# Performance work log

Measured on AMD Instinct MI355X. Metric: run time of the kernel, lower is better.

The kernel has to match this reference:

```python
import jax, jax.numpy as jnp
import numpy as np

EPS = 1e-5

def _layernorm(x, gamma, beta):
    mu = jnp.mean(x, axis=-1, keepdims=True)
    var = jnp.mean(jnp.square(x - mu), axis=-1, keepdims=True)
    return (x - mu) * jax.lax.rsqrt(var + EPS) * gamma + beta


def setup_inputs() -> dict:
    key = jax.random.key(0)
    ks = jax.random.split(key, 10)
    B, T, D, D1, F = 16, 256, 256, 64, 1024
    x = jax.random.normal(ks[0], (B, T, D), dtype=jnp.float32)
    U1 = jax.random.normal(ks[1], (B, T, T, D1), dtype=jnp.float32)
    mask = jnp.ones((B, T), dtype=bool)
    s = lambda fan_in: 1.0 / np.sqrt(fan_in)
    return {
        "x": x,
        "U1": U1,
        "mask": mask,
        "ln_mia_g": jnp.ones((D,), jnp.float32),
        "ln_mia_b": jnp.zeros((D,), jnp.float32),
        "Wv": jax.random.normal(ks[2], (D, D1), jnp.float32) * s(D),
        "Wo": jax.random.normal(ks[3], (D1, D), jnp.float32) * s(D1),
        "ln_ffn_g": jnp.ones((D,), jnp.float32),
        "ln_ffn_b": jnp.zeros((D,), jnp.float32),
        "W1": jax.random.normal(ks[4], (D, F), jnp.float32) * s(D),
        "b1": jnp.zeros((F,), jnp.float32),
        "W2": jax.random.normal(ks[5], (F, D), jnp.float32) * s(F),
        "b2": jnp.zeros((D,), jnp.float32),
    }


def reference(x, U1, mask, ln_mia_g, ln_mia_b, Wv, Wo, ln_ffn_g, ln_ffn_b, W1, b1, W2, b2):
    # MIA: per-channel softmax over source tokens j of external logits U1
    x_norm = _layernorm(x, ln_mia_g, ln_mia_b)          # [B,T,D]
    V = jnp.einsum('btd,de->bte', x_norm, Wv)           # [B,T,D1]
    # mask[b,j] False -> suppress source token j for all queries i, channels c
    logits = jnp.where(mask[:, None, :, None], U1, -jnp.inf)  # [B,T,T,D1]
    attn = jax.nn.softmax(logits, axis=2)               # softmax over j
    mia_out = jnp.einsum('bijc,bjc->bic', attn, V)      # [B,T,D1]
    x = x + jnp.einsum('btc,cd->btd', mia_out, Wo)
    # FFN (pre-norm), exact GELU as in torch nn.GELU default
    h = _layernorm(x, ln_ffn_g, ln_ffn_b)
    h = jax.nn.gelu(h @ W1 + b1, approximate=False) @ W2 + b2
    return x + h
```

## Files before the change

kernel.cpp:

```cpp
#include <hip/hip_runtime.h>
#include <math.h>

#define LNEPS 1e-5f

typedef short bf16x8 __attribute__((ext_vector_type(8)));
typedef float f32x4 __attribute__((ext_vector_type(4)));

__device__ __forceinline__ unsigned short f2bf(float f) {
    union { float f; unsigned int u; } v; v.f = f;
    unsigned int r = v.u + 0x7fffu + ((v.u >> 16) & 1u);
    return (unsigned short)(r >> 16);
}

__device__ __forceinline__ void block_ln_stats(float v, int tid, float* red,
                                               float& mu, float& rs) {
    float s = v, ss = v * v;
#pragma unroll
    for (int off = 32; off; off >>= 1) {
        s += __shfl_xor(s, off);
        ss += __shfl_xor(ss, off);
    }
    if ((tid & 63) == 0) { red[tid >> 6] = s; red[4 + (tid >> 6)] = ss; }
    __syncthreads();
    s = red[0] + red[1] + red[2] + red[3];
    ss = red[4] + red[5] + red[6] + red[7];
    mu = s * (1.0f / 256.0f);
    float var = ss * (1.0f / 256.0f) - mu * mu;
    rs = rsqrtf(var + LNEPS);
}

__device__ __forceinline__ float gelu_exact(float v) {
    return 0.5f * v * (1.0f + erff(v * 0.70710678118654752f));
}

__global__ __launch_bounds__(256) void kATT(const float* __restrict__ x,
                                            const float* __restrict__ g,
                                            const float* __restrict__ be,
                                            const float* __restrict__ Wv,
                                            float* __restrict__ V,
                                            const float* __restrict__ W1,
                                            unsigned short* __restrict__ W1t,
                                            const float* __restrict__ W2,
                                            unsigned short* __restrict__ W2t) {
    __shared__ float smem[32 * 33];
    const int bid = blockIdx.x, tid = threadIdx.x;
    if (bid < 4096) {
        float* sx = smem;
        float* red = smem + 256;
        float* part = smem + 264;
        const int token = bid;
        float v = x[(size_t)token * 256 + tid];
        float mu, rs;
        block_ln_stats(v, tid, red, mu, rs);
        sx[tid] = (v - mu) * rs * g[tid] + be[tid];
        __syncthreads();
        const int c = tid & 63, q = tid >> 6;
        float p = 0.f;
        const float* wp = Wv + (size_t)(q * 64) * 64 + c;
#pragma unroll 8
        for (int d = 0; d < 64; ++d) p = fmaf(sx[q * 64 + d], wp[(size_t)d * 64], p);
        part[q * 64 + c] = p;
        __syncthreads();
        if (tid < 64)
            V[(size_t)token * 64 + tid] =
                part[tid] + part[64 + tid] + part[128 + tid] + part[192 + tid];
    } else {
        int b = bid - 4096;
        const float* W;
        unsigned short* Wt;
        int K, N, n0, k0;
        if (b < 256) { W = W1; Wt = W1t; K = 256; N = 1024; n0 = (b & 31) * 32; k0 = (b >> 5) * 32; }
        else { b -= 256; W = W2; Wt = W2t; K = 1024; N = 256; n0 = (b & 7) * 32; k0 = (b >> 3) * 32; }
        float(*s)[33] = (float(*)[33])smem;
        const int cl = tid & 31, rq = tid >> 5;
#pragma unroll
        for (int i = 0; i < 4; ++i)
            s[rq * 4 + i][cl] = W[(size_t)(k0 + rq * 4 + i) * N + n0 + cl];
        __syncthreads();
#pragma unroll
        for (int i = 0; i < 4; ++i)
            Wt[(size_t)(n0 + rq * 4 + i) * K + k0 + cl] = f2bf(s[cl][rq * 4 + i]);
    }
}

__global__ __launch_bounds__(256) void kB(const float* __restrict__ x,
                                          const float4* __restrict__ U4,
                                          const int* __restrict__ mask,
                                          const float4* __restrict__ V4,
                                          const float* __restrict__ Wo,
                                          const float* __restrict__ gf,
                                          const float* __restrict__ bf,
                                          const float* __restrict__ b2,
                                          float* __restrict__ out,
                                          unsigned short* __restrict__ xn2b) {
    __shared__ float sl[16][64], al[16][64];
    __shared__ float mia[64];
    __shared__ float red[8];
    __shared__ float mkf[256];
    const int token = blockIdx.x, tid = threadIdx.x;
    const int b = token >> 8;
    const int l16 = tid & 15, jo = tid >> 4;
    mkf[tid] = (mask[b * 256 + tid] != 0) ? 1.0f : 0.0f;
    __syncthreads();

    float s0 = 0, s1 = 0, s2 = 0, s3 = 0;
    float a0 = 0, a1 = 0, a2 = 0, a3 = 0;
    const size_t ub = (size_t)token * (256 * 16);
    const size_t vb = (size_t)b * (256 * 16);
#pragma unroll 4
    for (int j = jo; j < 256; j += 16) {
        float4 u = U4[ub + (size_t)j * 16 + l16];
        float4 vv = V4[vb + (size_t)j * 16 + l16];
        float mw = mkf[j];
        float w;
        w = __expf(u.x) * mw; s0 += w; a0 = fmaf(w, vv.x, a0);
        w = __expf(u.y) * mw; s1 += w; a1 = fmaf(w, vv.y, a1);
        w = __expf(u.z) * mw; s2 += w; a2 = fmaf(w, vv.z, a2);
        w = __expf(u.w) * mw; s3 += w; a3 = fmaf(w, vv.w, a3);
    }
    sl[jo][l16 * 4 + 0] = s0; sl[jo][l16 * 4 + 1] = s1;
    sl[jo][l16 * 4 + 2] = s2; sl[jo][l16 * 4 + 3] = s3;
    al[jo][l16 * 4 + 0] = a0; al[jo][l16 * 4 + 1] = a1;
    al[jo][l16 * 4 + 2] = a2; al[jo][l16 * 4 + 3] = a3;
    __syncthreads();
    if (tid < 64) {
        float S = 0, A = 0;
#pragma unroll
        for (int p = 0; p < 16; ++p) { S += sl[p][tid]; A += al[p][tid]; }
        mia[tid] = A / S;
    }
    __syncthreads();

    float r = x[(size_t)token * 256 + tid];
#pragma unroll 8
    for (int c = 0; c < 64; ++c) r = fmaf(mia[c], Wo[(size_t)c * 256 + tid], r);
    out[(size_t)token * 256 + tid] = r + b2[tid];
    float mu, rs;
    block_ln_stats(r, tid, red, mu, rs);
    xn2b[(size_t)token * 256 + tid] = f2bf((r - mu) * rs * gf[tid] + bf[tid]);
}

__global__ __launch_bounds__(256) void kC2m(const unsigned short* __restrict__ A,
                                            const unsigned short* __restrict__ Bt,
                                            const float* __restrict__ b1,
                                            unsigned short* __restrict__ Aact) {
    __shared__ __align__(16) unsigned short As[128][72];
    __shared__ __align__(16) unsigned short Bs[64][72];
    const int tid = threadIdx.x;
    const int tileM = blockIdx.y * 128, tileN = blockIdx.x * 64;
    const int w = tid >> 6, lane = tid & 63;
    const int waveM = w >> 1, waveN = w & 1;
    const int fr = lane & 15, fg = lane >> 4;
    f32x4 acc[4][2] = {};
    for (int kc = 0; kc < 256; kc += 64) {
#pragma unroll
        for (int h = 0; h < 4; ++h) {
            int idx = tid + h * 256;
            int row = idx >> 3, seg = idx & 7;
            *(uint4*)&As[row][seg * 8] =
                *(const uint4*)&A[(size_t)(tileM + row) * 256 + kc + seg * 8];
        }
#pragma unroll
        for (int h = 0; h < 2; ++h) {
            int idx = tid + h * 256;
            int row = idx >> 3, seg = idx & 7;
            *(uint4*)&Bs[row][seg * 8] =
                *(const uint4*)&Bt[(size_t)(tileN + row) * 256 + kc + seg * 8];
        }
        __syncthreads();
        bf16x8 a[4][2], b[2][2];
#pragma unroll
        for (int m = 0; m < 4; ++m)
#pragma unroll
            for (int k = 0; k < 2; ++k)
                a[m][k] = *(const bf16x8*)&As[waveM * 64 + m * 16 + fr][k * 32 + fg * 8];
#pragma unroll
        for (int n = 0; n < 2; ++n)
#pragma unroll
            for (int k = 0; k < 2; ++k)
                b[n][k] = *(const bf16x8*)&Bs[waveN * 32 + n * 16 + fr][k * 32 + fg * 8];
#pragma unroll
        for (int k = 0; k < 2; ++k)
#pragma unroll
            for (int m = 0; m < 4; ++m)
#pragma unroll
                for (int n = 0; n < 2; ++n)
                    acc[m][n] = __builtin_amdgcn_mfma_f32_16x16x32_bf16(
                        a[m][k], b[n][k], acc[m][n], 0, 0, 0);
        __syncthreads();
    }
#pragma unroll
    for (int m = 0; m < 4; ++m)
#pragma unroll
        for (int n = 0; n < 2; ++n) {
            int col = tileN + waveN * 32 + n * 16 + fr;
            float bb = b1[col];
#pragma unroll
            for (int r = 0; r < 4; ++r) {
                int row = tileM + waveM * 64 + m * 16 + fg * 4 + r;
                float v = acc[m][n][r] + bb;
                Aact[(size_t)row * 1024 + col] = f2bf(gelu_exact(v));
            }
        }
}

__global__ __launch_bounds__(256) void kC3m(const unsigned short* __restrict__ A,
                                            const unsigned short* __restrict__ Bt,
                                            float* __restrict__ out) {
    __shared__ __align__(16) unsigned short As[64][72];
    __shared__ __align__(16) unsigned short Bs[64][72];
    const int tid = threadIdx.x;
    const int tileM = blockIdx.y * 64, tileN = blockIdx.x * 64;
    const int k0 = blockIdx.z * 512;
    const int w = tid >> 6, lane = tid & 63;
    const int waveM = w >> 1, waveN = w & 1;
    const int fr = lane & 15, fg = lane >> 4;
    f32x4 acc[2][2] = {};
    for (int kc = k0; kc < k0 + 512; kc += 64) {
#pragma unroll
        for (int h = 0; h < 2; ++h) {
            int idx = tid + h * 256;
            int row = idx >> 3, seg = idx & 7;
            *(uint4*)&As[row][seg * 8] =
                *(const uint4*)&A[(size_t)(tileM + row) * 1024 + kc + seg * 8];
        }
#pragma unroll
        for (int h = 0; h < 2; ++h) {
            int idx = tid + h * 256;
            int row = idx >> 3, seg = idx & 7;
            *(uint4*)&Bs[row][seg * 8] =
                *(const uint4*)&Bt[(size_t)(tileN + row) * 1024 + kc + seg * 8];
        }
        __syncthreads();
        bf16x8 a[2][2], b[2][2];
#pragma unroll
        for (int m = 0; m < 2; ++m)
#pragma unroll
            for (int k = 0; k < 2; ++k)
                a[m][k] = *(const bf16x8*)&As[waveM * 32 + m * 16 + fr][k * 32 + fg * 8];
#pragma unroll
        for (int n = 0; n < 2; ++n)
#pragma unroll
            for (int k = 0; k < 2; ++k)
                b[n][k] = *(const bf16x8*)&Bs[waveN * 32 + n * 16 + fr][k * 32 + fg * 8];
#pragma unroll
        for (int k = 0; k < 2; ++k)
#pragma unroll
            for (int m = 0; m < 2; ++m)
#pragma unroll
                for (int n = 0; n < 2; ++n)
                    acc[m][n] = __builtin_amdgcn_mfma_f32_16x16x32_bf16(
                        a[m][k], b[n][k], acc[m][n], 0, 0, 0);
        __syncthreads();
    }
#pragma unroll
    for (int m = 0; m < 2; ++m)
#pragma unroll
        for (int n = 0; n < 2; ++n) {
            int col = tileN + waveN * 32 + n * 16 + fr;
#pragma unroll
            for (int r = 0; r < 4; ++r) {
                int row = tileM + waveM * 32 + m * 16 + fg * 4 + r;
                atomicAdd(&out[(size_t)row * 256 + col], acc[m][n][r]);
            }
        }
}

extern "C" void kernel_launch(void* const* d_in, const int* in_sizes, int n_in,
                              void* d_out, int out_size, void* d_ws, size_t ws_size,
                              hipStream_t stream) {
    const float* x = (const float*)d_in[0];
    const float* U1 = (const float*)d_in[1];
    const int* mask = (const int*)d_in[2];
    const float* ln_mia_g = (const float*)d_in[3];
    const float* ln_mia_b = (const float*)d_in[4];
    const float* Wv = (const float*)d_in[5];
    const float* Wo = (const float*)d_in[6];
    const float* ln_ffn_g = (const float*)d_in[7];
    const float* ln_ffn_b = (const float*)d_in[8];
    const float* W1 = (const float*)d_in[9];
    const float* b1 = (const float*)d_in[10];
    const float* W2 = (const float*)d_in[11];
    const float* b2 = (const float*)d_in[12];
    float* out = (float*)d_out;

    char* ws = (char*)d_ws;
    float* V             = (float*)(ws);
    unsigned short* xn2b = (unsigned short*)(ws + (1u << 20));
    unsigned short* W1t  = (unsigned short*)(ws + (3u << 20));
    unsigned short* W2t  = (unsigned short*)(ws + (3u << 20) + (512u << 10));
    unsigned short* Aact = (unsigned short*)(ws + (4u << 20));

    kATT<<<4608, 256, 0, stream>>>(x, ln_mia_g, ln_mia_b, Wv, V, W1, W1t, W2, W2t);
    kB<<<4096, 256, 0, stream>>>(x, (const float4*)U1, mask, (const float4*)V,
                                 Wo, ln_ffn_g, ln_ffn_b, b2, out, xn2b);
    kC2m<<<dim3(16, 32), 256, 0, stream>>>(xn2b, W1t, b1, Aact);
    kC3m<<<dim3(4, 64, 2), 256, 0, stream>>>(Aact, W2t, out);
}
```

Before: 97.04 us.

## Fuse FFN up-projection, GELU and down-projection into one kernel

Replaces the two FFN GEMM kernels with one fused kernel. Each block handles 16 tokens and loops over 64-wide hidden chunks, computing the W1 product, bias and GELU into shared memory and accumulating the W2 product in registers. This removes the bf16 activation round trip through global memory, one kernel launch, and the atomic adds. In exchange only 256 blocks launch, and every block reloads all of W1 and W2 from global or L2, so there is much less parallelism and more weight traffic per token.

```diff
diff --git a/kernel.cpp b/kernel.cpp
--- a/kernel.cpp
+++ b/kernel.cpp
@@ -140,130 +140,85 @@
     xn2b[(size_t)token * 256 + tid] = f2bf((r - mu) * rs * gf[tid] + bf[tid]);
 }
 
-__global__ __launch_bounds__(256) void kC2m(const unsigned short* __restrict__ A,
-                                            const unsigned short* __restrict__ Bt,
+__global__ __launch_bounds__(256) void kFFN(const unsigned short* __restrict__ xn2b,
+                                            const unsigned short* __restrict__ W1t,
+                                            const unsigned short* __restrict__ W2t,
                                             const float* __restrict__ b1,
-                                            unsigned short* __restrict__ Aact) {
-    __shared__ __align__(16) unsigned short As[128][72];
-    __shared__ __align__(16) unsigned short Bs[64][72];
+                                            float* __restrict__ out) {
+    __shared__ __align__(16) unsigned short sXn[16][264];
+    __shared__ __align__(16) unsigned short sW1[64][264];
+    __shared__ __align__(16) unsigned short sW2[256][72];
+    __shared__ __align__(16) unsigned short sH[16][72];
     const int tid = threadIdx.x;
-    const int tileM = blockIdx.y * 128, tileN = blockIdx.x * 64;
+    const int t0 = blockIdx.x * 16;
     const int w = tid >> 6, lane = tid & 63;
-    const int waveM = w >> 1, waveN = w & 1;
     const int fr = lane & 15, fg = lane >> 4;
-    f32x4 acc[4][2] = {};
-    for (int kc = 0; kc < 256; kc += 64) {
-#pragma unroll
-        for (int h = 0; h < 4; ++h) {
+
+#pragma unroll
+    for (int h = 0; h < 2; ++h) {
+        int idx = tid + h * 256;
+        int row = idx >> 5, seg = idx & 31;
+        *(uint4*)&sXn[row][seg * 8] =
+            *(const uint4*)&xn2b[(size_t)(t0 + row) * 256 + seg * 8];
+    }
+
+    f32x4 acc2[4] = {};
+    for (int ch = 0; ch < 16; ++ch) {
+        const int c0 = ch * 64;
+#pragma unroll
+        for (int h = 0; h < 8; ++h) {
+            int idx = tid + h * 256;
+            int row = idx >> 5, seg = idx & 31;
+            *(uint4*)&sW1[row][seg * 8] =
+                *(const uint4*)&W1t[(size_t)(c0 + row) * 256 + seg * 8];
+        }
+#pragma unroll
+        for (int h = 0; h < 8; ++h) {
             int idx = tid + h * 256;
             int row = idx >> 3, seg = idx & 7;
-            *(uint4*)&As[row][seg * 8] =
-                *(const uint4*)&A[(size_t)(tileM + row) * 256 + kc + seg * 8];
-        }
-#pragma unroll
-        for (int h = 0; h < 2; ++h) {
-            int idx = tid + h * 256;
-            int row = idx >> 3, seg = idx & 7;
-            *(uint4*)&Bs[row][seg * 8] =
-                *(const uint4*)&Bt[(size_t)(tileN + row) * 256 + kc + seg * 8];
-        }
-        __syncthreads();
-        bf16x8 a[4][2], b[2][2];
-#pragma unroll
-        for (int m = 0; m < 4; ++m)
-#pragma unroll
-            for (int k = 0; k < 2; ++k)
-                a[m][k] = *(const bf16x8*)&As[waveM * 64 + m * 16 + fr][k * 32 + fg * 8];
-#pragma unroll
-        for (int n = 0; n < 2; ++n)
-#pragma unroll
-            for (int k = 0; k < 2; ++k)
-                b[n][k] = *(const bf16x8*)&Bs[waveN * 32 + n * 16 + fr][k * 32 + fg * 8];
-#pragma unroll
-        for (int k = 0; k < 2; ++k)
-#pragma unroll
-            for (int m = 0; m < 4; ++m)
-#pragma unroll
-                for (int n = 0; n < 2; ++n)
-                    acc[m][n] = __builtin_amdgcn_mfma_f32_16x16x32_bf16(
-                        a[m][k], b[n][k], acc[m][n], 0, 0, 0);
-        __syncthreads();
-    }
-#pragma unroll
-    for (int m = 0; m < 4; ++m)
-#pragma unroll
-        for (int n = 0; n < 2; ++n) {
-            int col = tileN + waveN * 32 + n * 16 + fr;
-            float bb = b1[col];
-#pragma unroll
-            for (int r = 0; r < 4; ++r) {
-                int row = tileM + waveM * 64 + m * 16 + fg * 4 + r;
-                float v = acc[m][n][r] + bb;
-                Aact[(size_t)row * 1024 + col] = f2bf(gelu_exact(v));
+            *(uint4*)&sW2[row][seg * 8] =
+                *(const uint4*)&W2t[(size_t)row * 1024 + c0 + seg * 8];
+        }
+        __syncthreads();
+
+        f32x4 h1a = {}, h1b = {};
+#pragma unroll
+        for (int ks = 0; ks < 8; ks += 2) {
+            bf16x8 a0 = *(const bf16x8*)&sXn[fr][ks * 32 + fg * 8];
+            bf16x8 b0 = *(const bf16x8*)&sW1[w * 16 + fr][ks * 32 + fg * 8];
+            bf16x8 a1 = *(const bf16x8*)&sXn[fr][(ks + 1) * 32 + fg * 8];
+            bf16x8 b1f = *(const bf16x8*)&sW1[w * 16 + fr][(ks + 1) * 32 + fg * 8];
+            h1a = __builtin_amdgcn_mfma_f32_16x16x32_bf16(a0, b0, h1a, 0, 0, 0);
+            h1b = __builtin_amdgcn_mfma_f32_16x16x32_bf16(a1, b1f, h1b, 0, 0, 0);
+        }
+        float bb = b1[c0 + w * 16 + fr];
+#pragma unroll
+        for (int r = 0; r < 4; ++r)
+            sH[fg * 4 + r][w * 16 + fr] = f2bf(gelu_exact(h1a[r] + h1b[r] + bb));
+        __syncthreads();
+
+#pragma unroll
+        for (int k2 = 0; k2 < 2; ++k2) {
+            bf16x8 a = *(const bf16x8*)&sH[fr][k2 * 32 + fg * 8];
+#pragma unroll
+            for (int q = 0; q < 4; ++q) {
+                bf16x8 b = *(const bf16x8*)&sW2[w * 64 + q * 16 + fr][k2 * 32 + fg * 8];
+                acc2[q] = __builtin_amdgcn_mfma_f32_16x16x32_bf16(a, b, acc2[q], 0, 0, 0);
             }
         }
-}
-
-__global__ __launch_bounds__(256) void kC3m(const unsigned short* __restrict__ A,
-                                            const unsigned short* __restrict__ Bt,
-                                            float* __restrict__ out) {
-    __shared__ __align__(16) unsigned short As[64][72];
-    __shared__ __align__(16) unsigned short Bs[64][72];
-    const int tid = threadIdx.x;
-    const int tileM = blockIdx.y * 64, tileN = blockIdx.x * 64;
-    const int k0 = blockIdx.z * 512;
-    const int w = tid >> 6, lane = tid & 63;
-    const int waveM = w >> 1, waveN = w & 1;
-    const int fr = lane & 15, fg = lane >> 4;
-    f32x4 acc[2][2] = {};
-    for (int kc = k0; kc < k0 + 512; kc += 64) {
-#pragma unroll
-        for (int h = 0; h < 2; ++h) {
-            int idx = tid + h * 256;
-            int row = idx >> 3, seg = idx & 7;
-            *(uint4*)&As[row][seg * 8] =
-                *(const uint4*)&A[(size_t)(tileM + row) * 1024 + kc + seg * 8];
-        }
-#pragma unroll
-        for (int h = 0; h < 2; ++h) {
-            int idx = tid + h * 256;
-            int row = idx >> 3, seg = idx & 7;
-            *(uint4*)&Bs[row][seg * 8] =
-                *(const uint4*)&Bt[(size_t)(tileN + row) * 1024 + kc + seg * 8];
-        }
-        __syncthreads();
-        bf16x8 a[2][2], b[2][2];
-#pragma unroll
-        for (int m = 0; m < 2; ++m)
-#pragma unroll
-            for (int k = 0; k < 2; ++k)
-                a[m][k] = *(const bf16x8*)&As[waveM * 32 + m * 16 + fr][k * 32 + fg * 8];
-#pragma unroll
-        for (int n = 0; n < 2; ++n)
-#pragma unroll
-            for (int k = 0; k < 2; ++k)
-                b[n][k] = *(const bf16x8*)&Bs[waveN * 32 + n * 16 + fr][k * 32 + fg * 8];
-#pragma unroll
-        for (int k = 0; k < 2; ++k)
-#pragma unroll
-            for (int m = 0; m < 2; ++m)
-#pragma unroll
-                for (int n = 0; n < 2; ++n)
-                    acc[m][n] = __builtin_amdgcn_mfma_f32_16x16x32_bf16(
-                        a[m][k], b[n][k], acc[m][n], 0, 0, 0);
-        __syncthreads();
-    }
-#pragma unroll
-    for (int m = 0; m < 2; ++m)
-#pragma unroll
-        for (int n = 0; n < 2; ++n) {
-            int col = tileN + waveN * 32 + n * 16 + fr;
-#pragma unroll
-            for (int r = 0; r < 4; ++r) {
-                int row = tileM + waveM * 32 + m * 16 + fg * 4 + r;
-                atomicAdd(&out[(size_t)row * 256 + col], acc[m][n][r]);
-            }
-        }
+        __syncthreads();
+    }
+
+#pragma unroll
+    for (int q = 0; q < 4; ++q) {
+        int col = w * 64 + q * 16 + fr;
+#pragma unroll
+        for (int r = 0; r < 4; ++r) {
+            int row = t0 + fg * 4 + r;
+            size_t idx = (size_t)row * 256 + col;
+            out[idx] += acc2[q][r];
+        }
+    }
 }
 
 extern "C" void kernel_launch(void* const* d_in, const int* in_sizes, int n_in,
@@ -289,11 +244,9 @@
     unsigned short* xn2b = (unsigned short*)(ws + (1u << 20));
     unsigned short* W1t  = (unsigned short*)(ws + (3u << 20));
     unsigned short* W2t  = (unsigned short*)(ws + (3u << 20) + (512u << 10));
-    unsigned short* Aact = (unsigned short*)(ws + (4u << 20));
 
     kATT<<<4608, 256, 0, stream>>>(x, ln_mia_g, ln_mia_b, Wv, V, W1, W1t, W2, W2t);
     kB<<<4096, 256, 0, stream>>>(x, (const float4*)U1, mask, (const float4*)V,
                                  Wo, ln_ffn_g, ln_ffn_b, b2, out, xn2b);
-    kC2m<<<dim3(16, 32), 256, 0, stream>>>(xn2b, W1t, b1, Aact);
-    kC3m<<<dim3(4, 64, 2), 256, 0, stream>>>(Aact, W2t, out);
-}
+    kFFN<<<256, 256, 0, stream>>>(xn2b, W1t, W2t, b1, out);
+}
```

Result: slower. 103.0 us (+6.1%).

## Batch 8 tokens per block in V projection and store V, Wo as bf16

Applied to the files above, without the earlier changes.

The V projection kernel now handles 8 tokens per block, with a 32-lane LayerNorm per token, so each Wv load is reused across 8 rows. V is written as bf16, and Wo is converted to bf16 by extra blocks in the same launch. The attention kernel then reads half-width V and Wo, cutting global and L2 traffic on its secondary streams. U1 stays fp32 and dominates that kernel's traffic. bf16 rounding of V and Wo adds some precision loss.

```diff
diff --git a/kernel.cpp b/kernel.cpp
--- a/kernel.cpp
+++ b/kernel.cpp
@@ -10,6 +10,12 @@
     union { float f; unsigned int u; } v; v.f = f;
     unsigned int r = v.u + 0x7fffu + ((v.u >> 16) & 1u);
     return (unsigned short)(r >> 16);
+}
+
+__device__ __forceinline__ float bf2f(unsigned short u) {
+    union { unsigned int i; float f; } v;
+    v.i = ((unsigned int)u) << 16;
+    return v.f;
 }
 
 __device__ __forceinline__ void block_ln_stats(float v, int tid, float* red,
@@ -37,35 +43,67 @@
                                             const float* __restrict__ g,
                                             const float* __restrict__ be,
                                             const float* __restrict__ Wv,
-                                            float* __restrict__ V,
+                                            unsigned short* __restrict__ Vb,
                                             const float* __restrict__ W1,
                                             unsigned short* __restrict__ W1t,
                                             const float* __restrict__ W2,
-                                            unsigned short* __restrict__ W2t) {
-    __shared__ float smem[32 * 33];
+                                            unsigned short* __restrict__ W2t,
+                                            const float* __restrict__ Wo,
+                                            unsigned short* __restrict__ Wob) {
+    __shared__ float smem[4096];
     const int bid = blockIdx.x, tid = threadIdx.x;
-    if (bid < 4096) {
+    if (bid < 512) {
         float* sx = smem;
-        float* red = smem + 256;
-        float* part = smem + 264;
-        const int token = bid;
-        float v = x[(size_t)token * 256 + tid];
-        float mu, rs;
-        block_ln_stats(v, tid, red, mu, rs);
-        sx[tid] = (v - mu) * rs * g[tid] + be[tid];
+        float* part = smem + 2048;
+        const int t0 = bid * 8;
+        {
+            const int r = tid >> 5, lc = tid & 31;
+            const float* xr = x + (size_t)(t0 + r) * 256 + lc * 8;
+            float vv[8];
+            *(float4*)&vv[0] = *(const float4*)xr;
+            *(float4*)&vv[4] = *(const float4*)(xr + 4);
+            float s = 0.f, ss = 0.f;
+#pragma unroll
+            for (int i = 0; i < 8; ++i) { s += vv[i]; ss = fmaf(vv[i], vv[i], ss); }
+#pragma unroll
+            for (int off = 16; off; off >>= 1) {
+                s += __shfl_xor(s, off, 32);
+                ss += __shfl_xor(ss, off, 32);
+            }
+            float mu = s * (1.0f / 256.0f);
+            float var = ss * (1.0f / 256.0f) - mu * mu;
+            float rs = rsqrtf(var + LNEPS);
+            const int c0 = lc * 8;
+            float o[8];
+#pragma unroll
+            for (int i = 0; i < 8; ++i)
+                o[i] = (vv[i] - mu) * rs * g[c0 + i] + be[c0 + i];
+            *(float4*)&sx[r * 256 + c0] = *(float4*)&o[0];
+            *(float4*)&sx[r * 256 + c0 + 4] = *(float4*)&o[4];
+        }
         __syncthreads();
         const int c = tid & 63, q = tid >> 6;
-        float p = 0.f;
+        float p[8] = {};
         const float* wp = Wv + (size_t)(q * 64) * 64 + c;
+        const float* sxp = sx + q * 64;
 #pragma unroll 8
-        for (int d = 0; d < 64; ++d) p = fmaf(sx[q * 64 + d], wp[(size_t)d * 64], p);
-        part[q * 64 + c] = p;
-        __syncthreads();
-        if (tid < 64)
-            V[(size_t)token * 64 + tid] =
-                part[tid] + part[64 + tid] + part[128 + tid] + part[192 + tid];
-    } else {
-        int b = bid - 4096;
+        for (int d = 0; d < 64; ++d) {
+            float wv = wp[(size_t)d * 64];
+#pragma unroll
+            for (int r = 0; r < 8; ++r) p[r] = fmaf(sxp[r * 256 + d], wv, p[r]);
+        }
+#pragma unroll
+        for (int r = 0; r < 8; ++r) part[(q * 8 + r) * 64 + c] = p[r];
+        __syncthreads();
+        const int rr = tid >> 6;
+#pragma unroll
+        for (int rw = rr; rw < 8; rw += 4) {
+            float sum = part[(0 * 8 + rw) * 64 + c] + part[(1 * 8 + rw) * 64 + c] +
+                        part[(2 * 8 + rw) * 64 + c] + part[(3 * 8 + rw) * 64 + c];
+            Vb[(size_t)(t0 + rw) * 64 + c] = f2bf(sum);
+        }
+    } else if (bid < 1024) {
+        int b = bid - 512;
         const float* W;
         unsigned short* Wt;
         int K, N, n0, k0;
@@ -80,14 +118,23 @@
 #pragma unroll
         for (int i = 0; i < 4; ++i)
             Wt[(size_t)(n0 + rq * 4 + i) * K + k0 + cl] = f2bf(s[cl][rq * 4 + i]);
+    } else {
+        int i = ((bid - 1024) * 256 + tid) * 8;
+        float4 a = *(const float4*)&Wo[i];
+        float4 d = *(const float4*)&Wo[i + 4];
+        ushort4 o1, o2;
+        o1.x = f2bf(a.x); o1.y = f2bf(a.y); o1.z = f2bf(a.z); o1.w = f2bf(a.w);
+        o2.x = f2bf(d.x); o2.y = f2bf(d.y); o2.z = f2bf(d.z); o2.w = f2bf(d.w);
+        *(ushort4*)&Wob[i] = o1;
+        *(ushort4*)&Wob[i + 4] = o2;
     }
 }
 
 __global__ __launch_bounds__(256) void kB(const float* __restrict__ x,
                                           const float4* __restrict__ U4,
                                           const int* __restrict__ mask,
-                                          const float4* __restrict__ V4,
-                                          const float* __restrict__ Wo,
+                                          const ushort4* __restrict__ V4b,
+                                          const unsigned short* __restrict__ Wob,
                                           const float* __restrict__ gf,
                                           const float* __restrict__ bf,
                                           const float* __restrict__ b2,
@@ -110,13 +157,13 @@
 #pragma unroll 4
     for (int j = jo; j < 256; j += 16) {
         float4 u = U4[ub + (size_t)j * 16 + l16];
-        float4 vv = V4[vb + (size_t)j * 16 + l16];
+        ushort4 vv4 = V4b[vb + (size_t)j * 16 + l16];
         float mw = mkf[j];
         float w;
-        w = __expf(u.x) * mw; s0 += w; a0 = fmaf(w, vv.x, a0);
-        w = __expf(u.y) * mw; s1 += w; a1 = fmaf(w, vv.y, a1);
-        w = __expf(u.z) * mw; s2 += w; a2 = fmaf(w, vv.z, a2);
-        w = __expf(u.w) * mw; s3 += w; a3 = fmaf(w, vv.w, a3);
+        w = __expf(u.x) * mw; s0 += w; a0 = fmaf(w, bf2f(vv4.x), a0);
+        w = __expf(u.y) * mw; s1 += w; a1 = fmaf(w, bf2f(vv4.y), a1);
+        w = __expf(u.z) * mw; s2 += w; a2 = fmaf(w, bf2f(vv4.z), a2);
+        w = __expf(u.w) * mw; s3 += w; a3 = fmaf(w, bf2f(vv4.w), a3);
     }
     sl[jo][l16 * 4 + 0] = s0; sl[jo][l16 * 4 + 1] = s1;
     sl[jo][l16 * 4 + 2] = s2; sl[jo][l16 * 4 + 3] = s3;
@@ -133,7 +180,8 @@
 
     float r = x[(size_t)token * 256 + tid];
 #pragma unroll 8
-    for (int c = 0; c < 64; ++c) r = fmaf(mia[c], Wo[(size_t)c * 256 + tid], r);
+    for (int c = 0; c < 64; ++c)
+        r = fmaf(mia[c], bf2f(Wob[(size_t)c * 256 + tid]), r);
     out[(size_t)token * 256 + tid] = r + b2[tid];
     float mu, rs;
     block_ln_stats(r, tid, red, mu, rs);
@@ -285,15 +333,17 @@
     float* out = (float*)d_out;
 
     char* ws = (char*)d_ws;
-    float* V             = (float*)(ws);
+    unsigned short* Vb   = (unsigned short*)(ws);
     unsigned short* xn2b = (unsigned short*)(ws + (1u << 20));
     unsigned short* W1t  = (unsigned short*)(ws + (3u << 20));
     unsigned short* W2t  = (unsigned short*)(ws + (3u << 20) + (512u << 10));
-    unsigned short* Aact = (unsigned short*)(ws + (4u << 20));
-
-    kATT<<<4608, 256, 0, stream>>>(x, ln_mia_g, ln_mia_b, Wv, V, W1, W1t, W2, W2t);
-    kB<<<4096, 256, 0, stream>>>(x, (const float4*)U1, mask, (const float4*)V,
-                                 Wo, ln_ffn_g, ln_ffn_b, b2, out, xn2b);
+    unsigned short* Wob  = (unsigned short*)(ws + (4u << 20));
+    unsigned short* Aact = (unsigned short*)(ws + (5u << 20));
+
+    kATT<<<1032, 256, 0, stream>>>(x, ln_mia_g, ln_mia_b, Wv, Vb,
+                                   W1, W1t, W2, W2t, Wo, Wob);
+    kB<<<4096, 256, 0, stream>>>(x, (const float4*)U1, mask, (const ushort4*)Vb,
+                                 Wob, ln_ffn_g, ln_ffn_b, b2, out, xn2b);
     kC2m<<<dim3(16, 32), 256, 0, stream>>>(xn2b, W1t, b1, Aact);
     kC3m<<<dim3(4, 64, 2), 256, 0, stream>>>(Aact, W2t, out);
 }
```

Result: faster. 82.16 us (-15.3%).
